# Optimization experiments

Measured on AMD Instinct MI355X. Metric: run time of the kernel, lower is better.

## Reference

```python
import jax, jax.numpy as jnp
import numpy as np

B, N, D = 8, 4096, 2


def setup_inputs() -> dict:
    key = jax.random.key(0)
    k1, k2 = jax.random.split(key)
    y_true = jax.random.normal(k1, (B, N, D), dtype=jnp.float32)
    y_pred = jax.random.normal(k2, (B, N, D), dtype=jnp.float32)
    return {"y_true": y_true, "y_pred": y_pred}


def reference(y_true, y_pred):
    # Bidirectional Chamfer distance (chamferdist semantics):
    # squared-Euclidean NN distances, sum over points, mean over batch, both directions.
    xx = jnp.sum(y_true * y_true, axis=-1)                      # [B, N]
    yy = jnp.sum(y_pred * y_pred, axis=-1)                      # [B, N]
    xy = jnp.einsum('bnd,bmd->bnm', y_true, y_pred)             # [B, N, N]
    d2 = jnp.maximum(xx[:, :, None] + yy[:, None, :] - 2.0 * xy, 0.0)  # [B, N, N]
    cd_fwd = jnp.mean(jnp.sum(jnp.min(d2, axis=2), axis=1))     # true -> pred
    cd_bwd = jnp.mean(jnp.sum(jnp.min(d2, axis=1), axis=1))     # pred -> true
    # EMD approximation: cumsum over the last (coordinate) axis, squared diff, mean.
    emd = jnp.mean(jnp.mean(jnp.square(jnp.cumsum(y_true, axis=-1) - jnp.cumsum(y_pred, axis=-1)), axis=-1))
    return cd_fwd + cd_bwd + emd
```

## Files before the change

kernel.cpp:

```cpp
#include <hip/hip_runtime.h>
#include <math.h>

#define BB    8
#define NN    4096
#define DIRS  2
#define TPB   256
#define Q     16
#define RSIZE 64
#define RC    (NN / RSIZE)
#define CDN   (DIRS * BB * NN)

__global__ __launch_bounds__(TPB, 4) void chamfer_kernel(
    const float* __restrict__ y_true, const float* __restrict__ y_pred,
    float* __restrict__ part, float* __restrict__ out)
{
    __shared__ float4 sxy[RSIZE / 2];
    __shared__ float2 sz [RSIZE / 2];

    const int rc  = blockIdx.x;
    const int dir = blockIdx.y;
    const int b   = blockIdx.z;
    const int t   = threadIdx.x;

    const float2* qbase  = (const float2*)(dir == 0 ? y_true : y_pred) + (size_t)b * NN;
    const float4* rbase4 = (const float4*)((dir == 0 ? y_pred : y_true) + (size_t)b * NN * 2);

    if (t < RSIZE / 2) {
        float4 r = rbase4[rc * (RSIZE / 2) + t];
        sxy[t] = make_float4(-2.f * r.x, -2.f * r.y, -2.f * r.z, -2.f * r.w);
        sz [t] = make_float2(r.x * r.x + r.y * r.y, r.z * r.z + r.w * r.w);
    }
    if (rc == 0 && dir == 0 && b == 0 && t == 0) out[0] = 0.f;
    __syncthreads();

    float qx[Q], qy[Q], m[Q];
    #pragma unroll
    for (int j = 0; j < Q; ++j) {
        float2 qv = qbase[j * TPB + t];
        qx[j] = qv.x; qy[j] = qv.y; m[j] = INFINITY;
    }

    #pragma unroll 2
    for (int k = 0; k < RSIZE / 2; ++k) {
        float4 xy = sxy[k];
        float2 z  = sz [k];
        #pragma unroll
        for (int j = 0; j < Q; ++j) {
            float d0 = fmaf(qy[j], xy.y, fmaf(qx[j], xy.x, z.x));
            float d1 = fmaf(qy[j], xy.w, fmaf(qx[j], xy.z, z.y));
            m[j] = fminf(m[j], d0);
            m[j] = fminf(m[j], d1);
        }
    }

    #pragma unroll
    for (int j = 0; j < Q; ++j) {
        int q = j * TPB + t;
        float v = fmaxf(m[j] + fmaf(qx[j], qx[j], qy[j] * qy[j]), 0.f);
        part[(size_t)rc * CDN + ((size_t)dir * BB + b) * NN + q] = v;
    }
}

__global__ __launch_bounds__(TPB) void reduce_kernel(
    const float* __restrict__ y_true, const float* __restrict__ y_pred,
    const float* __restrict__ part, float* __restrict__ out)
{
    const float cd_scale  = 1.0f / (float)BB;
    const float emd_scale = 1.0f / (2.0f * (float)BB * (float)NN);

    const int i = blockIdx.x * TPB + threadIdx.x;

    float mv = part[i];
    #pragma unroll 16
    for (int r = 1; r < RC; ++r)
        mv = fminf(mv, part[(size_t)r * CDN + i]);
    float acc = mv * cd_scale;

    if (i < BB * NN) {
        float2 tv = ((const float2*)y_true)[i];
        float2 pv = ((const float2*)y_pred)[i];
        float c1 = tv.x - pv.x;
        float c2 = c1 + (tv.y - pv.y);
        acc = fmaf(c1 * emd_scale, c1, acc);
        acc = fmaf(c2 * emd_scale, c2, acc);
    }

    #pragma unroll
    for (int off = 32; off > 0; off >>= 1)
        acc += __shfl_down(acc, off, 64);

    __shared__ float wsum[TPB / 64];
    const int lane = threadIdx.x & 63, wid = threadIdx.x >> 6;
    if (lane == 0) wsum[wid] = acc;
    __syncthreads();
    if (threadIdx.x == 0) {
        float s = wsum[0] + wsum[1] + wsum[2] + wsum[3];
        atomicAdd(out, s);
    }
}

extern "C" void kernel_launch(void* const* d_in, const int* in_sizes, int n_in,
                              void* d_out, int out_size, void* d_ws, size_t ws_size,
                              hipStream_t stream) {
    const float* y_true = (const float*)d_in[0];
    const float* y_pred = (const float*)d_in[1];
    float* out  = (float*)d_out;
    float* part = (float*)d_ws;

    chamfer_kernel<<<dim3(RC, DIRS, BB), TPB, 0, stream>>>(y_true, y_pred, part, out);
    reduce_kernel<<<CDN / TPB, TPB, 0, stream>>>(y_true, y_pred, part, out);
}
```

Measured before the change: 92.84 us.

## Vectorize chamfer inner loop with packed 2-wide FMA/min and larger reference tiles

```diff
diff --git a/kernel.cpp b/kernel.cpp
--- a/kernel.cpp
+++ b/kernel.cpp
@@ -6,16 +6,31 @@
 #define DIRS  2
 #define TPB   256
 #define Q     16
-#define RSIZE 64
+#define RSIZE 128
 #define RC    (NN / RSIZE)
 #define CDN   (DIRS * BB * NN)
 
-__global__ __launch_bounds__(TPB, 4) void chamfer_kernel(
+typedef float v2f __attribute__((ext_vector_type(2)));
+typedef float v4f __attribute__((ext_vector_type(4)));
+
+#if __has_builtin(__builtin_elementwise_fma) && __has_builtin(__builtin_elementwise_min)
+#define VFMA(a,b,c) __builtin_elementwise_fma(a,b,c)
+#define VMIN(a,b)   __builtin_elementwise_min(a,b)
+#else
+static __device__ inline v2f VFMA(v2f a, v2f b, v2f c) {
+    v2f r; r.x = fmaf(a.x,b.x,c.x); r.y = fmaf(a.y,b.y,c.y); return r;
+}
+static __device__ inline v2f VMIN(v2f a, v2f b) {
+    v2f r; r.x = fminf(a.x,b.x); r.y = fminf(a.y,b.y); return r;
+}
+#endif
+
+__global__ __launch_bounds__(TPB) void chamfer_kernel(
     const float* __restrict__ y_true, const float* __restrict__ y_pred,
     float* __restrict__ part, float* __restrict__ out)
 {
-    __shared__ float4 sxy[RSIZE / 2];
-    __shared__ float2 sz [RSIZE / 2];
+    __shared__ v4f sxy[RSIZE / 2];
+    __shared__ v2f sz [RSIZE / 2];
 
     const int rc  = blockIdx.x;
     const int dir = blockIdx.y;
@@ -27,36 +42,45 @@
 
     if (t < RSIZE / 2) {
         float4 r = rbase4[rc * (RSIZE / 2) + t];
-        sxy[t] = make_float4(-2.f * r.x, -2.f * r.y, -2.f * r.z, -2.f * r.w);
-        sz [t] = make_float2(r.x * r.x + r.y * r.y, r.z * r.z + r.w * r.w);
+        v4f xy; xy.x = -2.f * r.x; xy.y = -2.f * r.z;
+                xy.z = -2.f * r.y; xy.w = -2.f * r.w;
+        sxy[t] = xy;
+        v2f z;  z.x = fmaf(r.x, r.x, r.y * r.y);
+                z.y = fmaf(r.z, r.z, r.w * r.w);
+        sz[t] = z;
     }
     if (rc == 0 && dir == 0 && b == 0 && t == 0) out[0] = 0.f;
     __syncthreads();
 
-    float qx[Q], qy[Q], m[Q];
+    float qx[Q], qy[Q];
+    v2f   m2[Q];
     #pragma unroll
     for (int j = 0; j < Q; ++j) {
         float2 qv = qbase[j * TPB + t];
-        qx[j] = qv.x; qy[j] = qv.y; m[j] = INFINITY;
+        qx[j] = qv.x; qy[j] = qv.y;
+        m2[j].x = INFINITY; m2[j].y = INFINITY;
     }
 
     #pragma unroll 2
     for (int k = 0; k < RSIZE / 2; ++k) {
-        float4 xy = sxy[k];
-        float2 z  = sz [k];
+        v4f xy = sxy[k];
+        v2f z  = sz [k];
+        v2f rx = xy.xy;
+        v2f ry = xy.zw;
         #pragma unroll
         for (int j = 0; j < Q; ++j) {
-            float d0 = fmaf(qy[j], xy.y, fmaf(qx[j], xy.x, z.x));
-            float d1 = fmaf(qy[j], xy.w, fmaf(qx[j], xy.z, z.y));
-            m[j] = fminf(m[j], d0);
-            m[j] = fminf(m[j], d1);
+            v2f qxv = (v2f)(qx[j]);
+            v2f qyv = (v2f)(qy[j]);
+            v2f d = VFMA(ry, qyv, VFMA(rx, qxv, z));
+            m2[j] = VMIN(m2[j], d);
         }
     }
 
     #pragma unroll
     for (int j = 0; j < Q; ++j) {
         int q = j * TPB + t;
-        float v = fmaxf(m[j] + fmaf(qx[j], qx[j], qy[j] * qy[j]), 0.f);
+        float m = fminf(m2[j].x, m2[j].y);
+        float v = fmaxf(m + fmaf(qx[j], qx[j], qy[j] * qy[j]), 0.f);
         part[(size_t)rc * CDN + ((size_t)dir * BB + b) * NN + q] = v;
     }
 }
@@ -71,7 +95,7 @@
     const int i = blockIdx.x * TPB + threadIdx.x;
 
     float mv = part[i];
-    #pragma unroll 16
+    #pragma unroll 8
     for (int r = 1; r < RC; ++r)
         mv = fminf(mv, part[(size_t)r * CDN + i]);
     float acc = mv * cd_scale;
```

Result: faster. 81.51 us (-12.2%).
